# Kernel tuning notes

Measured on AMD Instinct MI355X. Metric: run time of the kernel, lower is better.

## Reference

```python
import jax, jax.numpy as jnp
import numpy as np

B, S, D = 2, 2048, 2048
H = 16
Q_LORA, KV_LORA = 1536, 512
ROPE_DIM, NOPE_DIM, V_DIM = 64, 64, 128
Q_HEAD_DIM = NOPE_DIM + ROPE_DIM  # 128
ROPE_THETA, ROPE_RATIO = 10000.0, 1.0


def setup_inputs() -> dict:
    key = jax.random.key(0)
    ks = jax.random.split(key, 6)
    std = 0.02
    return {
        "hidden_states": jax.random.normal(ks[0], (B, S, D), jnp.float32),
        "Wqa": jax.random.normal(ks[1], (D, Q_LORA), jnp.float32) * std,
        "Wqb": jax.random.normal(ks[2], (Q_LORA, H * Q_HEAD_DIM), jnp.float32) * std,
        "Wkva": jax.random.normal(ks[3], (D, KV_LORA + ROPE_DIM), jnp.float32) * std,
        "Wkvb": jax.random.normal(ks[4], (KV_LORA, H * (NOPE_DIM + V_DIM)), jnp.float32) * std,
        "Wo": jax.random.normal(ks[5], (H * V_DIM, D), jnp.float32) * std,
    }


def _rope_tables(seq_len):
    half = ROPE_DIM // 2
    inv_freq = ROPE_RATIO / (ROPE_THETA ** (jnp.arange(half, dtype=jnp.float32) * 2.0 / ROPE_DIM))
    freqs = jnp.arange(seq_len, dtype=jnp.float32)[:, None] * inv_freq[None, :]  # [S, half]
    return jnp.cos(freqs), jnp.sin(freqs)


def _apply_rope(x, cos, sin):
    # interleaved even/odd rotation, matches torch stack+flatten
    x_even = x[..., 0::2]
    x_odd = x[..., 1::2]
    r_even = x_even * cos - x_odd * sin
    r_odd = x_odd * cos + x_even * sin
    return jnp.stack([r_even, r_odd], axis=-1).reshape(x.shape)


def reference(hidden_states, Wqa, Wqb, Wkva, Wkvb, Wo):
    b, s, _ = hidden_states.shape
    scale = Q_HEAD_DIM ** -0.5

    # query compression path
    q_latent = hidden_states @ Wqa                             # [B,S,Q_LORA]
    q = (q_latent @ Wqb).reshape(b, s, H, Q_HEAD_DIM)
    q = jnp.transpose(q, (0, 2, 1, 3))                          # [B,H,S,q_head_dim]
    q_nope, q_pe = q[..., :NOPE_DIM], q[..., NOPE_DIM:]

    # kv compression
    kv_comp = hidden_states @ Wkva                              # [B,S,KV_LORA+ROPE]
    c_kv, k_pe = kv_comp[..., :KV_LORA], kv_comp[..., KV_LORA:]

    cos, sin = _rope_tables(s)                                  # [S, ROPE_DIM//2]
    q_pe = _apply_rope(q_pe, cos, sin)                          # [B,H,S,ROPE]
    k_pe = _apply_rope(k_pe, cos, sin)                          # [B,S,ROPE]

    # kv decompression
    kv = (c_kv @ Wkvb).reshape(b, s, H, NOPE_DIM + V_DIM)
    kv = jnp.transpose(kv, (0, 2, 1, 3))                        # [B,H,S,nope+v]
    k_nope, v = kv[..., :NOPE_DIM], kv[..., NOPE_DIM:]

    k_pe_b = jnp.broadcast_to(k_pe[:, None], (b, H, s, ROPE_DIM))
    q_full = jnp.concatenate([q_nope, q_pe], axis=-1)           # [B,H,S,128]
    k_full = jnp.concatenate([k_nope, k_pe_b], axis=-1)         # [B,H,S,128]

    scores = jnp.einsum('bhqd,bhkd->bhqk', q_full, k_full) * scale
    causal = jnp.tril(jnp.ones((s, s), dtype=bool))
    scores = jnp.where(causal[None, None], scores, jnp.finfo(scores.dtype).min)
    probs = jax.nn.softmax(scores, axis=-1)
    attn = jnp.einsum('bhqk,bhkd->bhqd', probs, v)              # [B,H,S,V_DIM]

    out = jnp.transpose(attn, (0, 2, 1, 3)).reshape(b, s, H * V_DIM)
    return out @ Wo                                             # [B,S,D]
```

## Files before the change

kernel.cpp:

```cpp
#include <hip/hip_runtime.h>
#include <hip/hip_bf16.h>
#include <cstdint>
#include <cstddef>

typedef __bf16 bf16_t;
typedef __attribute__((ext_vector_type(8))) __bf16 bf16x8;
typedef __attribute__((ext_vector_type(4))) float f32x4;

#define S_ 2048
#define H_ 16
#define NTOK 4096

__device__ __forceinline__ f32x4 mfma16x16(bf16x8 a, bf16x8 b, f32x4 c) {
  return __builtin_amdgcn_mfma_f32_16x16x32_bf16(a, b, c, 0, 0, 0);
}
__device__ __forceinline__ bf16x8 load8(const bf16_t* p) {
  return *reinterpret_cast<const bf16x8*>(p);
}
__device__ __forceinline__ void load_lds16(const void* g, void* l) {
  __builtin_amdgcn_global_load_lds(
      (const __attribute__((address_space(1))) uint32_t*)g,
      (__attribute__((address_space(3))) uint32_t*)l, 16, 0, 0);
}


__global__ void cast_bf16_k(const float* __restrict__ in, bf16_t* __restrict__ out, int n) {
  int idx = blockIdx.x * 256 + threadIdx.x;
  int i4 = idx * 4;
  if (i4 >= n) return;
  float4 v = *reinterpret_cast<const float4*>(in + i4);
  out[i4 + 0] = (bf16_t)v.x;
  out[i4 + 1] = (bf16_t)v.y;
  out[i4 + 2] = (bf16_t)v.z;
  out[i4 + 3] = (bf16_t)v.w;
}

__global__ void transpose_cast_k(const float* __restrict__ in, bf16_t* __restrict__ out,
                                 int K, int Nsrc, int Nout) {
  __shared__ float tile[32][33];
  int k0 = blockIdx.y * 32, n0 = blockIdx.x * 32;
  int tx = threadIdx.x & 31, ty = threadIdx.x >> 5;
#pragma unroll
  for (int i = 0; i < 4; ++i) {
    int k = k0 + ty + i * 8, n = n0 + tx;
    tile[ty + i * 8][tx] = (n < Nsrc) ? in[(size_t)k * Nsrc + n] : 0.0f;
  }
  __syncthreads();
#pragma unroll
  for (int i = 0; i < 4; ++i) {
    int n = n0 + ty + i * 8, k = k0 + tx;
    out[(size_t)n * K + k] = (bf16_t)tile[tx][ty + i * 8];
  }
}

__global__ void transpose_v_k(const bf16_t* __restrict__ kv, bf16_t* __restrict__ vT) {
  __shared__ bf16_t tile[32][33];
  int bh = blockIdx.z;
  int b = bh >> 4, h = bh & 15;
  int s0 = blockIdx.x * 32, d0 = blockIdx.y * 32;
  int tx = threadIdx.x & 31, ty = threadIdx.x >> 5;
#pragma unroll
  for (int i = 0; i < 4; ++i) {
    int s = s0 + ty + i * 8;
    tile[ty + i * 8][tx] = kv[(size_t)(b * S_ + s) * 3072 + h * 192 + 64 + d0 + tx];
  }
  __syncthreads();
#pragma unroll
  for (int i = 0; i < 4; ++i) {
    int d = d0 + ty + i * 8;
    vT[((size_t)bh * 128 + d) * 2048 + s0 + tx] = tile[tx][ty + i * 8];
  }
}

__global__ void rope_tables_k(float* __restrict__ cosT, float* __restrict__ sinT) {
  int idx = blockIdx.x * 256 + threadIdx.x;
  if (idx >= S_ * 32) return;
  int s = idx >> 5, i = idx & 31;
  float inv = powf(10000.0f, -(2.0f * (float)i) / 64.0f);
  float fr = (float)s * inv;
  cosT[idx] = cosf(fr);
  sinT[idx] = sinf(fr);
}

__global__ void rope_apply_k(bf16_t* __restrict__ buf, const float* __restrict__ cosT,
                             const float* __restrict__ sinT, int ld, int nh, int hstride, int off) {
  int idx = blockIdx.x * 256 + threadIdx.x;
  int total = NTOK * nh * 32;
  if (idx >= total) return;
  int i = idx & 31;
  int h = (idx >> 5) % nh;
  int t = idx / (32 * nh);
  int s = t & (S_ - 1);
  float c = cosT[s * 32 + i], sn = sinT[s * 32 + i];
  bf16_t* p = buf + (size_t)t * ld + off + h * hstride + 2 * i;
  float xe = (float)p[0], xo = (float)p[1];
  p[0] = (bf16_t)(xe * c - xo * sn);
  p[1] = (bf16_t)(xo * c + xe * sn);
}


template <int OUT_F32>
__global__ __launch_bounds__(256) void gemm_bf16(const bf16_t* __restrict__ A, int lda,
                                                 const bf16_t* __restrict__ Bt,
                                                 void* __restrict__ Cv, int M, int N, int K,
                                                 float scale) {
  __shared__ alignas(16) bf16_t Al[128 * 32];
  __shared__ alignas(16) bf16_t Bl[128 * 32];
  const int tid = threadIdx.x;
  const int wid = tid >> 6, lane = tid & 63;
  const int m0 = blockIdx.y * 128, n0 = blockIdx.x * 128;
  const int wm = (wid >> 1) * 64, wn = (wid & 1) * 64;

  f32x4 acc[4][4] = {};

  const int srow = wid * 32 + (lane >> 2);
  const int scol = (lane & 3) * 8;
  const bf16_t* ag0 = A + (size_t)(m0 + srow) * lda + scol;
  const bf16_t* ag1 = A + (size_t)(m0 + srow + 16) * lda + scol;
  const bf16_t* bg0 = Bt + (size_t)(n0 + srow) * K + scol;
  const bf16_t* bg1 = Bt + (size_t)(n0 + srow + 16) * K + scol;
  bf16_t* al0 = &Al[wid * 1024];
  bf16_t* al1 = &Al[wid * 1024 + 512];
  bf16_t* bl0 = &Bl[wid * 1024];
  bf16_t* bl1 = &Bl[wid * 1024 + 512];

  const int lr = lane & 15, lk = (lane >> 4) * 8;

  for (int k0 = 0; k0 < K; k0 += 32) {
    load_lds16(ag0 + k0, al0);
    load_lds16(ag1 + k0, al1);
    load_lds16(bg0 + k0, bl0);
    load_lds16(bg1 + k0, bl1);
    __syncthreads();
    bf16x8 af[4], bfr[4];
#pragma unroll
    for (int i = 0; i < 4; ++i) {
      af[i] = load8(&Al[(wm + i * 16 + lr) * 32 + lk]);
      bfr[i] = load8(&Bl[(wn + i * 16 + lr) * 32 + lk]);
    }
#pragma unroll
    for (int i = 0; i < 4; ++i)
#pragma unroll
      for (int j = 0; j < 4; ++j) acc[i][j] = mfma16x16(af[i], bfr[j], acc[i][j]);
    __syncthreads();
  }

  const int lg = lane >> 4;
  if (OUT_F32) {
    float* C = (float*)Cv;
#pragma unroll
    for (int i = 0; i < 4; ++i)
#pragma unroll
      for (int j = 0; j < 4; ++j)
#pragma unroll
        for (int r = 0; r < 4; ++r) {
          int row = m0 + wm + i * 16 + lg * 4 + r;
          int col = n0 + wn + j * 16 + lr;
          C[(size_t)row * N + col] = acc[i][j][r] * scale;
        }
  } else {
    bf16_t* C = (bf16_t*)Cv;
#pragma unroll
    for (int i = 0; i < 4; ++i)
#pragma unroll
      for (int j = 0; j < 4; ++j)
#pragma unroll
        for (int r = 0; r < 4; ++r) {
          int row = m0 + wm + i * 16 + lg * 4 + r;
          int col = n0 + wn + j * 16 + lr;
          C[(size_t)row * N + col] = (bf16_t)(acc[i][j][r] * scale);
        }
  }
}

__global__ __launch_bounds__(256) void attn_fused(const bf16_t* __restrict__ q,
                                                  const bf16_t* __restrict__ kv,
                                                  const bf16_t* __restrict__ lat,
                                                  const bf16_t* __restrict__ vT,
                                                  bf16_t* __restrict__ out) {
  __shared__ alignas(16) bf16_t Kn[64 * 64];
  __shared__ alignas(16) bf16_t Kp[64 * 64];
  __shared__ alignas(16) bf16_t Vt[128 * 64];
  __shared__ alignas(16) bf16_t Pl[4 * 16 * 64];
  const int tid = threadIdx.x, wid = tid >> 6, lane = tid & 63;
  const int bid = blockIdx.x;
  const int pairi = bid >> 5;
  const int bh = bid & 31;
  const int b = bh >> 4, h = bh & 15;
  const int tokb = b * S_;
  const int lr = lane & 15, lg = lane >> 4;
  const int srow8 = lane >> 3, c8 = lane & 7;
  const int swz8 = c8 ^ srow8;
  bf16_t* Pw = &Pl[wid * 1024];

  for (int phase = 0; phase < 2; ++phase) {
    const int qt = phase ? (31 - pairi) : pairi;

    bf16x8 qf[4];
    {
      const int qrow = qt * 64 + wid * 16 + lr;
      const bf16_t* qp = q + (size_t)(tokb + qrow) * 2048 + h * 128 + lg * 8;
#pragma unroll
      for (int ds = 0; ds < 4; ++ds) qf[ds] = load8(qp + ds * 32);
    }

    f32x4 o[8] = {};
    float mrow[4] = {-1e30f, -1e30f, -1e30f, -1e30f};
    float lrow[4] = {0.f, 0.f, 0.f, 0.f};

    for (int t = 0; t <= qt; ++t) {
      const int kb = t * 64;
#pragma unroll
      for (int rr = 0; rr < 2; ++rr) {
        const int r0 = wid * 16 + rr * 8;
        const int row = r0 + srow8;
        const size_t tk = (size_t)(tokb + kb + row);
        load_lds16(kv + tk * 3072 + h * 192 + (swz8 << 3), &Kn[r0 * 64]);
        load_lds16(lat + tk * 2176 + 2048 + (swz8 << 3), &Kp[r0 * 64]);
      }
#pragma unroll
      for (int rr = 0; rr < 4; ++rr) {
        const int r0 = wid * 32 + rr * 8;
        const int row = r0 + srow8;
        load_lds16(vT + ((size_t)bh * 128 + row) * 2048 + kb + (swz8 << 3), &Vt[r0 * 64]);
      }
      __syncthreads();

      f32x4 s[4];
#pragma unroll
      for (int kt = 0; kt < 4; ++kt) {
        const int row = kt * 16 + lr;
        const int e = lr & 7;
        bf16x8 kf0 = load8(&Kn[row * 64 + ((lg ^ e) << 3)]);
        bf16x8 kf1 = load8(&Kn[row * 64 + (((lg + 4) ^ e) << 3)]);
        bf16x8 kf2 = load8(&Kp[row * 64 + ((lg ^ e) << 3)]);
        bf16x8 kf3 = load8(&Kp[row * 64 + (((lg + 4) ^ e) << 3)]);
        f32x4 acc = {0.f, 0.f, 0.f, 0.f};
        acc = mfma16x16(qf[0], kf0, acc);
        acc = mfma16x16(qf[1], kf1, acc);
        acc = mfma16x16(qf[2], kf2, acc);
        acc = mfma16x16(qf[3], kf3, acc);
        s[kt] = acc;
      }

      if (t == qt) {
#pragma unroll
        for (int kt = 0; kt < 4; ++kt) {
          const int key = kb + kt * 16 + lr;
#pragma unroll
          for (int r = 0; r < 4; ++r) {
            const int qr = qt * 64 + wid * 16 + lg * 4 + r;
            if (key > qr) s[kt][r] = -1e30f;
          }
        }
      }

      float corr[4];
#pragma unroll
      for (int r = 0; r < 4; ++r) {
        float mx = fmaxf(fmaxf(s[0][r], s[1][r]), fmaxf(s[2][r], s[3][r]));
        mx = fmaxf(mx, __shfl_xor(mx, 1));
        mx = fmaxf(mx, __shfl_xor(mx, 2));
        mx = fmaxf(mx, __shfl_xor(mx, 4));
        mx = fmaxf(mx, __shfl_xor(mx, 8));
        float mn = fmaxf(mrow[r], mx);
        corr[r] = __expf(mrow[r] - mn);
        mrow[r] = mn;
      }
      float psum[4] = {0.f, 0.f, 0.f, 0.f};
#pragma unroll
      for (int kt = 0; kt < 4; ++kt)
#pragma unroll
        for (int r = 0; r < 4; ++r) {
          float p = __expf(s[kt][r] - mrow[r]);
          s[kt][r] = p;
          psum[r] += p;
        }
#pragma unroll
      for (int r = 0; r < 4; ++r) {
        float ps = psum[r];
        ps += __shfl_xor(ps, 1);
        ps += __shfl_xor(ps, 2);
        ps += __shfl_xor(ps, 4);
        ps += __shfl_xor(ps, 8);
        lrow[r] = lrow[r] * corr[r] + ps;
      }
#pragma unroll
      for (int n = 0; n < 8; ++n)
#pragma unroll
        for (int r = 0; r < 4; ++r) o[n][r] *= corr[r];

#pragma unroll
      for (int kt = 0; kt < 4; ++kt)
#pragma unroll
        for (int r = 0; r < 4; ++r) {
          const int qrow = lg * 4 + r;
          const int key = kt * 16 + lr;
          Pw[qrow * 64 + ((((key >> 3) ^ (qrow & 7)) << 3) | (key & 7))] = (bf16_t)s[kt][r];
        }

#pragma unroll
      for (int ks = 0; ks < 2; ++ks) {
        const int e = lr & 7;
        bf16x8 pa = load8(&Pw[lr * 64 + (((ks * 4 + lg) ^ e) << 3)]);
#pragma unroll
        for (int n = 0; n < 8; ++n) {
          bf16x8 vb = load8(&Vt[(n * 16 + lr) * 64 + (((ks * 4 + lg) ^ e) << 3)]);
          o[n] = mfma16x16(pa, vb, o[n]);
        }
      }
      __syncthreads();
    }

#pragma unroll
    for (int n = 0; n < 8; ++n)
#pragma unroll
      for (int r = 0; r < 4; ++r) {
        const int qr = qt * 64 + wid * 16 + lg * 4 + r;
        float val = o[n][r] / lrow[r];
        out[(size_t)(tokb + qr) * 2048 + h * 128 + n * 16 + lr] = (bf16_t)val;
      }
  }
}


extern "C" void kernel_launch(void* const* d_in, const int* in_sizes, int n_in, void* d_out,
                              int out_size, void* d_ws, size_t ws_size, hipStream_t stream) {
  const float* hs = (const float*)d_in[0];
  const float* Wqa = (const float*)d_in[1];
  const float* Wqb = (const float*)d_in[2];
  const float* Wkva = (const float*)d_in[3];
  const float* Wkvb = (const float*)d_in[4];
  const float* Wo = (const float*)d_in[5];
  float* out = (float*)d_out;

  char* ws = (char*)d_ws;
  size_t off = 0;
  auto alloc = [&](size_t bytes) {
    void* p = ws + off;
    off += (bytes + 255) & ~(size_t)255;
    return p;
  };
  bf16_t* hsb = (bf16_t*)alloc((size_t)NTOK * 2048 * 2);
  bf16_t* W1t = (bf16_t*)alloc((size_t)2176 * 2048 * 2);
  bf16_t* Wqbt = (bf16_t*)alloc((size_t)2048 * 1536 * 2);
  bf16_t* Wkvbt = (bf16_t*)alloc((size_t)3072 * 512 * 2);
  bf16_t* Wot = (bf16_t*)alloc((size_t)2048 * 2048 * 2);
  bf16_t* lat = (bf16_t*)alloc((size_t)NTOK * 2176 * 2);
  bf16_t* qb = (bf16_t*)alloc((size_t)NTOK * 2048 * 2);
  bf16_t* kvb = (bf16_t*)alloc((size_t)NTOK * 3072 * 2);
  bf16_t* attn = (bf16_t*)alloc((size_t)NTOK * 2048 * 2);
  bf16_t* vT = (bf16_t*)alloc((size_t)32 * 128 * 2048 * 2);
  float* cosT = (float*)alloc((size_t)S_ * 32 * 4);
  float* sinT = (float*)alloc((size_t)S_ * 32 * 4);

  cast_bf16_k<<<(NTOK * 2048 / 4 + 255) / 256, 256, 0, stream>>>(hs, hsb, NTOK * 2048);
  transpose_cast_k<<<dim3(1536 / 32, 2048 / 32), 256, 0, stream>>>(Wqa, W1t, 2048, 1536, 1536);
  transpose_cast_k<<<dim3(640 / 32, 2048 / 32), 256, 0, stream>>>(Wkva, W1t + (size_t)1536 * 2048,
                                                                  2048, 576, 640);
  transpose_cast_k<<<dim3(2048 / 32, 1536 / 32), 256, 0, stream>>>(Wqb, Wqbt, 1536, 2048, 2048);
  transpose_cast_k<<<dim3(3072 / 32, 512 / 32), 256, 0, stream>>>(Wkvb, Wkvbt, 512, 3072, 3072);
  transpose_cast_k<<<dim3(2048 / 32, 2048 / 32), 256, 0, stream>>>(Wo, Wot, 2048, 2048, 2048);
  rope_tables_k<<<(S_ * 32 + 255) / 256, 256, 0, stream>>>(cosT, sinT);

  gemm_bf16<0><<<dim3(2176 / 128, NTOK / 128), 256, 0, stream>>>(hsb, 2048, W1t, lat, NTOK, 2176,
                                                                 2048, 1.0f);
  rope_apply_k<<<(NTOK * 32 + 255) / 256, 256, 0, stream>>>(lat, cosT, sinT, 2176, 1, 0, 2048);
  const float scale = 0.08838834764831845f;
  gemm_bf16<0><<<dim3(2048 / 128, NTOK / 128), 256, 0, stream>>>(lat, 2176, Wqbt, qb, NTOK, 2048,
                                                                 1536, scale);
  rope_apply_k<<<(NTOK * 16 * 32 + 255) / 256, 256, 0, stream>>>(qb, cosT, sinT, 2048, 16, 128, 64);
  gemm_bf16<0><<<dim3(3072 / 128, NTOK / 128), 256, 0, stream>>>(lat + 1536, 2176, Wkvbt, kvb, NTOK,
                                                                 3072, 512, 1.0f);
  transpose_v_k<<<dim3(64, 4, 32), 256, 0, stream>>>(kvb, vT);
  attn_fused<<<dim3(512), 256, 0, stream>>>(qb, kvb, lat, vT, attn);
  gemm_bf16<1><<<dim3(2048 / 128, NTOK / 128), 256, 0, stream>>>(attn, 2048, Wot, out, NTOK, 2048,
                                                                 2048, 1.0f);
}
```

Baseline: 328.5 us.

## Double-buffer attention K/V tiles, lazy softmax rescale, exp2, wider GEMM K tile

The attention kernel now double-buffers the K-nope, K-rope and V tiles in LDS, so the next tile's loads are issued while the current one is computed. It sets MFMA phases to high wave priority, folds log2(e) into the Q scale so it can use exp2f, and skips the running-max rescale unless some row's max grows by more than 8. The GEMM kernel's K tile grows from 32 to 64, which halves the barriers per K step and doubles LDS use. The lazy rescale lets unnormalised exponentials reach up to 2^8 before the final division, which is fine in fp32 but can lose some bf16 precision in P.

```diff
diff --git a/kernel.cpp b/kernel.cpp
--- a/kernel.cpp
+++ b/kernel.cpp
@@ -104,8 +104,8 @@
                                                  const bf16_t* __restrict__ Bt,
                                                  void* __restrict__ Cv, int M, int N, int K,
                                                  float scale) {
-  __shared__ alignas(16) bf16_t Al[128 * 32];
-  __shared__ alignas(16) bf16_t Bl[128 * 32];
+  __shared__ alignas(16) bf16_t Al[128 * 64];
+  __shared__ alignas(16) bf16_t Bl[128 * 64];
   const int tid = threadIdx.x;
   const int wid = tid >> 6, lane = tid & 63;
   const int m0 = blockIdx.y * 128, n0 = blockIdx.x * 128;
@@ -113,39 +113,37 @@
 
   f32x4 acc[4][4] = {};
 
-  const int srow = wid * 32 + (lane >> 2);
-  const int scol = (lane & 3) * 8;
-  const bf16_t* ag0 = A + (size_t)(m0 + srow) * lda + scol;
-  const bf16_t* ag1 = A + (size_t)(m0 + srow + 16) * lda + scol;
-  const bf16_t* bg0 = Bt + (size_t)(n0 + srow) * K + scol;
-  const bf16_t* bg1 = Bt + (size_t)(n0 + srow + 16) * K + scol;
-  bf16_t* al0 = &Al[wid * 1024];
-  bf16_t* al1 = &Al[wid * 1024 + 512];
-  bf16_t* bl0 = &Bl[wid * 1024];
-  bf16_t* bl1 = &Bl[wid * 1024 + 512];
-
-  const int lr = lane & 15, lk = (lane >> 4) * 8;
-
-  for (int k0 = 0; k0 < K; k0 += 32) {
-    load_lds16(ag0 + k0, al0);
-    load_lds16(ag1 + k0, al1);
-    load_lds16(bg0 + k0, bl0);
-    load_lds16(bg1 + k0, bl1);
+  const int srow = lane >> 3;
+  const int scol = (lane & 7) * 8;
+  const bf16_t* agB = A + (size_t)(m0 + wid * 32 + srow) * lda + scol;
+  const bf16_t* bgB = Bt + (size_t)(n0 + wid * 32 + srow) * K + scol;
+
+  const int lr = lane & 15, lg = lane >> 4;
+
+  for (int k0 = 0; k0 < K; k0 += 64) {
+#pragma unroll
+    for (int rr = 0; rr < 4; ++rr) {
+      load_lds16(agB + (size_t)rr * 8 * lda + k0, &Al[(wid * 32 + rr * 8) * 64]);
+      load_lds16(bgB + (size_t)rr * 8 * K + k0, &Bl[(wid * 32 + rr * 8) * 64]);
+    }
     __syncthreads();
-    bf16x8 af[4], bfr[4];
-#pragma unroll
-    for (int i = 0; i < 4; ++i) {
-      af[i] = load8(&Al[(wm + i * 16 + lr) * 32 + lk]);
-      bfr[i] = load8(&Bl[(wn + i * 16 + lr) * 32 + lk]);
+#pragma unroll
+    for (int kk = 0; kk < 2; ++kk) {
+      bf16x8 af[4], bfr[4];
+#pragma unroll
+      for (int i = 0; i < 4; ++i) {
+        af[i] = load8(&Al[(wm + i * 16 + lr) * 64 + kk * 32 + lg * 8]);
+        bfr[i] = load8(&Bl[(wn + i * 16 + lr) * 64 + kk * 32 + lg * 8]);
+      }
+#pragma unroll
+      for (int i = 0; i < 4; ++i)
+#pragma unroll
+        for (int j = 0; j < 4; ++j) acc[i][j] = mfma16x16(af[i], bfr[j], acc[i][j]);
     }
-#pragma unroll
-    for (int i = 0; i < 4; ++i)
-#pragma unroll
-      for (int j = 0; j < 4; ++j) acc[i][j] = mfma16x16(af[i], bfr[j], acc[i][j]);
     __syncthreads();
   }
 
-  const int lg = lane >> 4;
+  const int lg2 = lane >> 4;
   if (OUT_F32) {
     float* C = (float*)Cv;
 #pragma unroll
@@ -154,7 +152,7 @@
       for (int j = 0; j < 4; ++j)
 #pragma unroll
         for (int r = 0; r < 4; ++r) {
-          int row = m0 + wm + i * 16 + lg * 4 + r;
+          int row = m0 + wm + i * 16 + lg2 * 4 + r;
           int col = n0 + wn + j * 16 + lr;
           C[(size_t)row * N + col] = acc[i][j][r] * scale;
         }
@@ -166,7 +164,7 @@
       for (int j = 0; j < 4; ++j)
 #pragma unroll
         for (int r = 0; r < 4; ++r) {
-          int row = m0 + wm + i * 16 + lg * 4 + r;
+          int row = m0 + wm + i * 16 + lg2 * 4 + r;
           int col = n0 + wn + j * 16 + lr;
           C[(size_t)row * N + col] = (bf16_t)(acc[i][j][r] * scale);
         }
@@ -178,10 +176,10 @@
                                                   const bf16_t* __restrict__ lat,
                                                   const bf16_t* __restrict__ vT,
                                                   bf16_t* __restrict__ out) {
-  __shared__ alignas(16) bf16_t Kn[64 * 64];
-  __shared__ alignas(16) bf16_t Kp[64 * 64];
-  __shared__ alignas(16) bf16_t Vt[128 * 64];
-  __shared__ alignas(16) bf16_t Pl[4 * 16 * 64];
+  __shared__ alignas(16) bf16_t Kn[2][64 * 64];
+  __shared__ alignas(16) bf16_t Kp[2][64 * 64];
+  __shared__ alignas(16) bf16_t Vt[2][128 * 64];
+  __shared__ alignas(16) bf16_t Pl[4][16 * 64];
   const int tid = threadIdx.x, wid = tid >> 6, lane = tid & 63;
   const int bid = blockIdx.x;
   const int pairi = bid >> 5;
@@ -191,7 +189,7 @@
   const int lr = lane & 15, lg = lane >> 4;
   const int srow8 = lane >> 3, c8 = lane & 7;
   const int swz8 = c8 ^ srow8;
-  bf16_t* Pw = &Pl[wid * 1024];
+  bf16_t* Pw = &Pl[wid][0];
 
   for (int phase = 0; phase < 2; ++phase) {
     const int qt = phase ? (31 - pairi) : pairi;
@@ -208,33 +206,40 @@
     float mrow[4] = {-1e30f, -1e30f, -1e30f, -1e30f};
     float lrow[4] = {0.f, 0.f, 0.f, 0.f};
 
-    for (int t = 0; t <= qt; ++t) {
+    auto STAGE = [&](int buf, int t) {
       const int kb = t * 64;
 #pragma unroll
       for (int rr = 0; rr < 2; ++rr) {
         const int r0 = wid * 16 + rr * 8;
-        const int row = r0 + srow8;
-        const size_t tk = (size_t)(tokb + kb + row);
-        load_lds16(kv + tk * 3072 + h * 192 + (swz8 << 3), &Kn[r0 * 64]);
-        load_lds16(lat + tk * 2176 + 2048 + (swz8 << 3), &Kp[r0 * 64]);
+        const size_t tk = (size_t)(tokb + kb + r0 + srow8);
+        load_lds16(kv + tk * 3072 + h * 192 + (swz8 << 3), &Kn[buf][r0 * 64]);
+        load_lds16(lat + tk * 2176 + 2048 + (swz8 << 3), &Kp[buf][r0 * 64]);
       }
 #pragma unroll
       for (int rr = 0; rr < 4; ++rr) {
         const int r0 = wid * 32 + rr * 8;
-        const int row = r0 + srow8;
-        load_lds16(vT + ((size_t)bh * 128 + row) * 2048 + kb + (swz8 << 3), &Vt[r0 * 64]);
-      }
-      __syncthreads();
+        load_lds16(vT + ((size_t)bh * 128 + r0 + srow8) * 2048 + kb + (swz8 << 3),
+                   &Vt[buf][r0 * 64]);
+      }
+    };
+
+    STAGE(0, 0);
+    __syncthreads();
+
+    for (int t = 0; t <= qt; ++t) {
+      const int cur = t & 1;
+      if (t < qt) STAGE(cur ^ 1, t + 1);
 
       f32x4 s[4];
+      __builtin_amdgcn_s_setprio(1);
 #pragma unroll
       for (int kt = 0; kt < 4; ++kt) {
         const int row = kt * 16 + lr;
         const int e = lr & 7;
-        bf16x8 kf0 = load8(&Kn[row * 64 + ((lg ^ e) << 3)]);
-        bf16x8 kf1 = load8(&Kn[row * 64 + (((lg + 4) ^ e) << 3)]);
-        bf16x8 kf2 = load8(&Kp[row * 64 + ((lg ^ e) << 3)]);
-        bf16x8 kf3 = load8(&Kp[row * 64 + (((lg + 4) ^ e) << 3)]);
+        bf16x8 kf0 = load8(&Kn[cur][row * 64 + ((lg ^ e) << 3)]);
+        bf16x8 kf1 = load8(&Kn[cur][row * 64 + (((lg + 4) ^ e) << 3)]);
+        bf16x8 kf2 = load8(&Kp[cur][row * 64 + ((lg ^ e) << 3)]);
+        bf16x8 kf3 = load8(&Kp[cur][row * 64 + (((lg + 4) ^ e) << 3)]);
         f32x4 acc = {0.f, 0.f, 0.f, 0.f};
         acc = mfma16x16(qf[0], kf0, acc);
         acc = mfma16x16(qf[1], kf1, acc);
@@ -242,8 +247,10 @@
         acc = mfma16x16(qf[3], kf3, acc);
         s[kt] = acc;
       }
+      __builtin_amdgcn_s_setprio(0);
 
       if (t == qt) {
+        const int kb = t * 64;
 #pragma unroll
         for (int kt = 0; kt < 4; ++kt) {
           const int key = kb + kt * 16 + lr;
@@ -255,7 +262,7 @@
         }
       }
 
-      float corr[4];
+      float tm[4];
 #pragma unroll
       for (int r = 0; r < 4; ++r) {
         float mx = fmaxf(fmaxf(s[0][r], s[1][r]), fmaxf(s[2][r], s[3][r]));
@@ -263,16 +270,27 @@
         mx = fmaxf(mx, __shfl_xor(mx, 2));
         mx = fmaxf(mx, __shfl_xor(mx, 4));
         mx = fmaxf(mx, __shfl_xor(mx, 8));
-        float mn = fmaxf(mrow[r], mx);
-        corr[r] = __expf(mrow[r] - mn);
-        mrow[r] = mn;
+        tm[r] = mx;
+      }
+      float need = fmaxf(fmaxf(tm[0] - mrow[0], tm[1] - mrow[1]),
+                         fmaxf(tm[2] - mrow[2], tm[3] - mrow[3]));
+      if (!__all(need <= 8.0f)) {
+#pragma unroll
+        for (int r = 0; r < 4; ++r) {
+          float mn = fmaxf(mrow[r], tm[r]);
+          float corr = exp2f(mrow[r] - mn);
+          mrow[r] = mn;
+          lrow[r] *= corr;
+#pragma unroll
+          for (int n = 0; n < 8; ++n) o[n][r] *= corr;
+        }
       }
       float psum[4] = {0.f, 0.f, 0.f, 0.f};
 #pragma unroll
       for (int kt = 0; kt < 4; ++kt)
 #pragma unroll
         for (int r = 0; r < 4; ++r) {
-          float p = __expf(s[kt][r] - mrow[r]);
+          float p = exp2f(s[kt][r] - mrow[r]);
           s[kt][r] = p;
           psum[r] += p;
         }
@@ -283,12 +301,8 @@
         ps += __shfl_xor(ps, 2);
         ps += __shfl_xor(ps, 4);
         ps += __shfl_xor(ps, 8);
-        lrow[r] = lrow[r] * corr[r] + ps;
-      }
-#pragma unroll
-      for (int n = 0; n < 8; ++n)
-#pragma unroll
-        for (int r = 0; r < 4; ++r) o[n][r] *= corr[r];
+        lrow[r] += ps;
+      }
 
 #pragma unroll
       for (int kt = 0; kt < 4; ++kt)
@@ -299,16 +313,18 @@
           Pw[qrow * 64 + ((((key >> 3) ^ (qrow & 7)) << 3) | (key & 7))] = (bf16_t)s[kt][r];
         }
 
+      __builtin_amdgcn_s_setprio(1);
 #pragma unroll
       for (int ks = 0; ks < 2; ++ks) {
         const int e = lr & 7;
         bf16x8 pa = load8(&Pw[lr * 64 + (((ks * 4 + lg) ^ e) << 3)]);
 #pragma unroll
         for (int n = 0; n < 8; ++n) {
-          bf16x8 vb = load8(&Vt[(n * 16 + lr) * 64 + (((ks * 4 + lg) ^ e) << 3)]);
+          bf16x8 vb = load8(&Vt[cur][(n * 16 + lr) * 64 + (((ks * 4 + lg) ^ e) << 3)]);
           o[n] = mfma16x16(pa, vb, o[n]);
         }
       }
+      __builtin_amdgcn_s_setprio(0);
       __syncthreads();
     }
 
@@ -366,7 +382,7 @@
   gemm_bf16<0><<<dim3(2176 / 128, NTOK / 128), 256, 0, stream>>>(hsb, 2048, W1t, lat, NTOK, 2176,
                                                                  2048, 1.0f);
   rope_apply_k<<<(NTOK * 32 + 255) / 256, 256, 0, stream>>>(lat, cosT, sinT, 2176, 1, 0, 2048);
-  const float scale = 0.08838834764831845f;
+  const float scale = 0.08838834764831845f * 1.4426950408889634f;
   gemm_bf16<0><<<dim3(2048 / 128, NTOK / 128), 256, 0, stream>>>(lat, 2176, Wqbt, qb, NTOK, 2048,
                                                                  1536, scale);
   rope_apply_k<<<(NTOK * 16 * 32 + 255) / 256, 256, 0, stream>>>(qb, cosT, sinT, 2048, 16, 128, 64);
```

New measurement: 341.4 us. +3.9%, slower.
